# Kernel tuning notes

Measured on AMD Instinct MI355X. Metric: run time of the kernel, lower is better.

## Reference

```python
import jax, jax.numpy as jnp
import numpy as np

FM = 32          # feature_maps
OUT_BITS = 16    # output_bits
PASS_STEPS = 3
N_EDGES = 3_200_000
VAR_COUNT = 100_000
CONST_COUNT = 50_000
EPS = 1e-5       # torch LayerNorm default


def _ln(x):
    # LayerNorm over last dim, elementwise_affine=False
    mu = jnp.mean(x, axis=-1, keepdims=True)
    var = jnp.mean((x - mu) ** 2, axis=-1, keepdims=True)
    return (x - mu) / jnp.sqrt(var + EPS)


def _mlp_ln(x, W1, b1, W2, b2):
    # Linear -> ReLU -> Linear -> LayerNorm(no affine)
    return _ln(jax.nn.relu(x @ W1 + b1) @ W2 + b2)


def _linear_init(key, fan_in, fan_out):
    kW, kb = jax.random.split(key)
    bound = 1.0 / np.sqrt(fan_in)
    W = jax.random.uniform(kW, (fan_in, fan_out), jnp.float32, -bound, bound)
    b = jax.random.uniform(kb, (fan_out,), jnp.float32, -bound, bound)
    return W, b


def setup_inputs() -> dict:
    key = jax.random.key(0)
    ks = jax.random.split(key, 12)
    inp = {}
    inp["edge_var"] = jax.random.randint(ks[0], (N_EDGES,), 0, VAR_COUNT, dtype=jnp.int64 if jax.config.jax_enable_x64 else jnp.int32)
    inp["edge_const"] = jax.random.randint(ks[1], (N_EDGES,), 0, CONST_COUNT, dtype=jnp.int64 if jax.config.jax_enable_x64 else jnp.int32)
    inp["edge_val"] = jax.random.normal(ks[2], (N_EDGES,), jnp.float32)
    inp["conditions_values"] = jax.random.normal(ks[3], (CONST_COUNT,), jnp.float32)
    inp["var_count"] = VAR_COUNT
    inp["const_count"] = CONST_COUNT
    # prepare_cond: 1 -> 2*fm -> fm
    inp["pc_W1"], inp["pc_b1"] = _linear_init(ks[4], 1, 2 * FM)
    inp["pc_W2"], inp["pc_b2"] = _linear_init(ks[5], 2 * FM, FM)
    # constraint_update: 3*fm -> 2*fm -> fm
    inp["cu_W1"], inp["cu_b1"] = _linear_init(ks[6], 3 * FM, 2 * FM)
    inp["cu_W2"], inp["cu_b2"] = _linear_init(ks[7], 2 * FM, FM)
    # variable_update: 2*fm -> 2*fm -> fm
    inp["vu_W1"], inp["vu_b1"] = _linear_init(ks[8], 2 * FM, 2 * FM)
    inp["vu_W2"], inp["vu_b2"] = _linear_init(ks[9], 2 * FM, FM)
    # output: fm -> 2*fm -> output_bits
    inp["out_W1"], inp["out_b1"] = _linear_init(ks[10], FM, 2 * FM)
    inp["out_W2"], inp["out_b2"] = _linear_init(ks[11], 2 * FM, OUT_BITS)
    return inp


def reference(edge_var, edge_const, edge_val, conditions_values, var_count, const_count,
              pc_W1, pc_b1, pc_W2, pc_b2,
              cu_W1, cu_b1, cu_W2, cu_b2,
              vu_W1, vu_b1, vu_W2, vu_b2,
              out_W1, out_b1, out_W2, out_b2):
    variables = jnp.ones((var_count, FM), dtype=edge_val.dtype)
    emb = _mlp_ln(conditions_values[:, None], pc_W1, pc_b1, pc_W2, pc_b2)  # [C, fm]
    constraints = emb
    ev = edge_val[:, None]
    for _ in range(PASS_STEPS):
        # adj.T @ variables : scatter-add variable features into constraints
        v2c = jax.ops.segment_sum(variables[edge_var] * ev, edge_const, num_segments=const_count)
        constraints = _mlp_ln(jnp.concatenate([constraints, emb, v2c], axis=-1),
                              cu_W1, cu_b1, cu_W2, cu_b2)
        # adj @ constraints : scatter-add constraint features into variables
        c2v = jax.ops.segment_sum(constraints[edge_const] * ev, edge_var, num_segments=var_count)
        variables = _mlp_ln(jnp.concatenate([variables, c2v], axis=-1),
                            vu_W1, vu_b1, vu_W2, vu_b2)
    out = jax.nn.relu(variables @ out_W1 + out_b1) @ out_W2 + out_b2
    return jax.nn.sigmoid(out)
```

## Files before the change

### kernel.cpp

```cpp
#include <hip/hip_runtime.h>
#include <hip/hip_fp16.h>
#include <math.h>

#define FM 32
#define N_EDGES 3200000
#define VAR_COUNT 100000
#define CONST_COUNT 50000
#define LN_EPS 1e-5f

#define EPB 4096
#define ABLK 782
#define NB 782
#define AB2 784
#define LSTRIDE 784
#define CAP 4608

typedef _Float16 f16;
typedef __attribute__((ext_vector_type(4))) _Float16 f16x4;
typedef __attribute__((ext_vector_type(4))) float f32x4;

static __device__ __forceinline__ float warp_sum32(float v) {
#pragma unroll
    for (int m = 16; m; m >>= 1) v += __shfl_xor(v, m);
    return v;
}

__global__ void init_vars(float* __restrict__ v, __half* __restrict__ v16, int n) {
    int i = blockIdx.x * 256 + threadIdx.x;
    if (i < n) {
        if (v) v[i] = 1.0f;
        if (v16) v16[i] = __float2half(1.0f);
    }
}


template <int DSHIFT>
__global__ __launch_bounds__(256) void bucket_sort(
    const int* __restrict__ dest_arr, const int* __restrict__ src_arr,
    const float* __restrict__ val_arr,
    int2* __restrict__ recs_tmp, int* __restrict__ lscan, int* __restrict__ rlen_T,
    int n) {
    __shared__ int hist[NB];
    __shared__ int cursor[NB];
    __shared__ int chunk[256];
    __shared__ int2 stage[EPB];
    const int t = threadIdx.x;
    const int base = blockIdx.x * EPB;
    const int nb = min(EPB, n - base);
    for (int i = t; i < NB; i += 256) hist[i] = 0;
    __syncthreads();
    int dg[16], pk[16], vb[16];
#pragma unroll
    for (int k = 0; k < 16; ++k) {
        int j = k * 256 + t;
        dg[k] = -1;
        if (j < nb) {
            int dest = dest_arr[base + j];
            int src  = src_arr[base + j];
            vb[k] = __float_as_int(val_arr[base + j]);
            dg[k] = dest >> DSHIFT;
            pk[k] = ((dest & ((1 << DSHIFT) - 1)) << 20) | src;
            atomicAdd(&hist[dg[k]], 1);
        }
    }
    __syncthreads();
    int sum = 0;
#pragma unroll
    for (int k = 0; k < 4; ++k) {
        int idx = t * 4 + k;
        if (idx < NB) sum += hist[idx];
    }
    chunk[t] = sum;
    __syncthreads();
    for (int off = 1; off < 256; off <<= 1) {
        int v = (t >= off) ? chunk[t - off] : 0;
        __syncthreads();
        chunk[t] += v;
        __syncthreads();
    }
    int run = chunk[t] - sum;
#pragma unroll
    for (int k = 0; k < 4; ++k) {
        int idx = t * 4 + k;
        if (idx < NB) {
            int h = hist[idx];
            rlen_T[(size_t)idx * AB2 + blockIdx.x] = h;
            hist[idx] = run;
            cursor[idx] = run;
            run += h;
        }
    }
    __syncthreads();
    {
        int* lp = lscan + (size_t)blockIdx.x * LSTRIDE;
        for (int i = t; i < NB; i += 256) lp[i] = hist[i];
        if (t == 0) lp[NB] = nb;
    }
#pragma unroll
    for (int k = 0; k < 16; ++k) {
        if (dg[k] >= 0) {
            int pos = atomicAdd(&cursor[dg[k]], 1);
            stage[pos] = make_int2(pk[k], vb[k]);
        }
    }
    __syncthreads();
    for (int j = t; j < nb; j += 256) recs_tmp[(size_t)base + j] = stage[j];
}

__global__ __launch_bounds__(256) void row_sum(const int* __restrict__ rlen_T,
                                               int* __restrict__ btot) {
    __shared__ int ls[256];
    const int t = threadIdx.x;
    const int* rp = rlen_T + (size_t)blockIdx.x * AB2;
    int s = 0;
    for (int b = t; b < ABLK; b += 256) s += rp[b];
    ls[t] = s;
    __syncthreads();
    for (int off = 128; off; off >>= 1) {
        if (t < off) ls[t] += ls[t + off];
        __syncthreads();
    }
    if (t == 0) btot[blockIdx.x] = ls[0];
}

__global__ __launch_bounds__(256) void scan_btot(
    const int* __restrict__ btot, int* __restrict__ bb, int n, int total) {
    __shared__ int ls[256];
    const int t = threadIdx.x;
    int idx = t * 4;
    int a0 = (idx + 0 < n) ? btot[idx + 0] : 0;
    int a1 = (idx + 1 < n) ? btot[idx + 1] : 0;
    int a2 = (idx + 2 < n) ? btot[idx + 2] : 0;
    int a3 = (idx + 3 < n) ? btot[idx + 3] : 0;
    int tsum = a0 + a1 + a2 + a3;
    ls[t] = tsum;
    __syncthreads();
    for (int off = 1; off < 256; off <<= 1) {
        int v = (t >= off) ? ls[t - off] : 0;
        __syncthreads();
        ls[t] += v;
        __syncthreads();
    }
    int excl = ls[t] - tsum;
    if (idx + 0 < n) bb[idx + 0] = excl;
    if (idx + 1 < n) bb[idx + 1] = excl + a0;
    if (idx + 2 < n) bb[idx + 2] = excl + a0 + a1;
    if (idx + 3 < n) bb[idx + 3] = excl + a0 + a1 + a2;
    if (t == 0) bb[n] = total;
}


template <int DSHIFT, int NDEST>
__global__ __launch_bounds__(256) void collect_sort(
    const int2* __restrict__ recs_tmp, const int* __restrict__ lscan,
    const int* __restrict__ rlen_T, const int* __restrict__ bb,
    int2* __restrict__ recs_out, int* __restrict__ offs,
    float* __restrict__ wsum, int nrows) {
    __shared__ int2 stage[CAP];
    __shared__ int rloff[256];
    __shared__ int hist[NDEST];
    __shared__ int cursor[NDEST];
    __shared__ int sc[NDEST];
    __shared__ float wsumL[NDEST];
    __shared__ int nb_s;
    const int t = threadIdx.x;
    const int k = blockIdx.x;
    const int b0 = t * 4;
    int s0 = 0, s1 = 0, s2 = 0, s3 = 0, l0 = 0, l1 = 0, l2 = 0, l3 = 0;
    if (b0 + 0 < ABLK) { s0 = lscan[(size_t)(b0 + 0) * LSTRIDE + k]; l0 = rlen_T[(size_t)k * AB2 + b0 + 0]; }
    if (b0 + 1 < ABLK) { s1 = lscan[(size_t)(b0 + 1) * LSTRIDE + k]; l1 = rlen_T[(size_t)k * AB2 + b0 + 1]; }
    if (b0 + 2 < ABLK) { s2 = lscan[(size_t)(b0 + 2) * LSTRIDE + k]; l2 = rlen_T[(size_t)k * AB2 + b0 + 2]; }
    if (b0 + 3 < ABLK) { s3 = lscan[(size_t)(b0 + 3) * LSTRIDE + k]; l3 = rlen_T[(size_t)k * AB2 + b0 + 3]; }
    int tsum = l0 + l1 + l2 + l3;
    rloff[t] = tsum;
    __syncthreads();
    for (int off = 1; off < 256; off <<= 1) {
        int v = (t >= off) ? rloff[t - off] : 0;
        __syncthreads();
        rloff[t] += v;
        __syncthreads();
    }
    if (t == 255) nb_s = rloff[255];
    int o0 = rloff[t] - tsum;
    int o1 = o0 + l0, o2 = o1 + l1, o3 = o2 + l2;
    for (int i = t; i < NDEST; i += 256) { hist[i] = 0; wsumL[i] = 0.0f; }
    __syncthreads();
    const int nb = min(nb_s, CAP);
    {
        const int2* rp = recs_tmp + (size_t)(b0 + 0) * EPB + s0;
        for (int j = 0; j < l0; ++j) if (o0 + j < CAP) stage[o0 + j] = rp[j];
        rp = recs_tmp + (size_t)(b0 + 1) * EPB + s1;
        for (int j = 0; j < l1; ++j) if (o1 + j < CAP) stage[o1 + j] = rp[j];
        rp = recs_tmp + (size_t)(b0 + 2) * EPB + s2;
        for (int j = 0; j < l2; ++j) if (o2 + j < CAP) stage[o2 + j] = rp[j];
        rp = recs_tmp + (size_t)(b0 + 3) * EPB + s3;
        for (int j = 0; j < l3; ++j) if (o3 + j < CAP) stage[o3 + j] = rp[j];
    }
    __syncthreads();
    for (int j = t; j < nb; j += 256) {
        int2 r = stage[j];
        atomicAdd(&hist[r.x >> 20], 1);
        if (wsum) atomicAdd(&wsumL[r.x >> 20], __int_as_float(r.y));
    }
    __syncthreads();
    if (t < NDEST) sc[t] = hist[t];
    __syncthreads();
    for (int off = 1; off < NDEST; off <<= 1) {
        int v = (t >= off && t < NDEST) ? sc[t - off] : 0;
        __syncthreads();
        if (t < NDEST) sc[t] += v;
        __syncthreads();
    }
    if (t < NDEST) {
        int excl = sc[t] - hist[t];
        cursor[t] = excl;
        int gd = (k << DSHIFT) + t;
        if (gd <= nrows) offs[gd] = bb[k] + excl;
        if (wsum && gd < nrows) wsum[gd] = wsumL[t];
    }
    __syncthreads();
    const int base_out = bb[k];
    for (int j = t; j < nb; j += 256) {
        int2 r = stage[j];
        int pos = atomicAdd(&cursor[r.x >> 20], 1);
        recs_out[(size_t)base_out + pos] = make_int2(r.x & 0xFFFFF, r.y);
    }
}


__global__ __launch_bounds__(256) void seg_gather16(
    const int* __restrict__ offs, const int2* __restrict__ recs,
    const __half* __restrict__ src16, __half* __restrict__ dst16, int nrows) {
    const int g = threadIdx.x >> 4, f2 = threadIdx.x & 15;
    const int row = blockIdx.x * 16 + g;
    if (row >= nrows) return;
    int j = offs[row];
    const int j1 = offs[row + 1];
    const __half2* __restrict__ s2 = (const __half2*)src16;
    float ax[8], ay[8];
#pragma unroll
    for (int u = 0; u < 8; ++u) { ax[u] = 0.0f; ay[u] = 0.0f; }
    for (; j + 8 <= j1; j += 8) {
        int2 r[8];
#pragma unroll
        for (int u = 0; u < 8; ++u) r[u] = recs[j + u];
        __half2 hh[8];
#pragma unroll
        for (int u = 0; u < 8; ++u) hh[u] = s2[(size_t)r[u].x * 16 + f2];
#pragma unroll
        for (int u = 0; u < 8; ++u) {
            float w = __int_as_float(r[u].y);
            float2 f = __half22float2(hh[u]);
            ax[u] = fmaf(f.x, w, ax[u]);
            ay[u] = fmaf(f.y, w, ay[u]);
        }
    }
    for (; j < j1; ++j) {
        int2 ra = recs[j];
        __half2 ha = s2[(size_t)ra.x * 16 + f2];
        float wa = __int_as_float(ra.y);
        float2 fa = __half22float2(ha);
        ax[0] = fmaf(fa.x, wa, ax[0]);
        ay[0] = fmaf(fa.y, wa, ay[0]);
    }
    float rx = ((ax[0] + ax[1]) + (ax[2] + ax[3])) + ((ax[4] + ax[5]) + (ax[6] + ax[7]));
    float ry = ((ay[0] + ay[1]) + (ay[2] + ay[3])) + ((ay[4] + ay[5]) + (ay[6] + ay[7]));
    ((__half2*)dst16)[(size_t)row * 16 + f2] = __floats2half2_rn(rx, ry);
}


__global__ __launch_bounds__(256) void scatter_edges(
    const int* __restrict__ src_idx, const int* __restrict__ dst_idx,
    const float* __restrict__ ev, const float* __restrict__ src,
    float* __restrict__ dst, int n_edges) {
    int e = blockIdx.x * 8 + (threadIdx.x >> 5);
    int f = threadIdx.x & 31;
    if (e >= n_edges) return;
    atomicAdd(&dst[(size_t)dst_idx[e] * FM + f], src[(size_t)src_idx[e] * FM + f] * ev[e]);
}


template <int NSEG>
__global__ __launch_bounds__(256) void mlp_mfma(
    const __half* __restrict__ s0h, const __half* __restrict__ s1h,
    const __half* __restrict__ s2h, const float* __restrict__ ws,
    const float* __restrict__ W1, const float* __restrict__ b1,
    const float* __restrict__ W2, const float* __restrict__ b2,
    __half* __restrict__ dst16, int nrows) {
    constexpr int KT = NSEG * 2;
    __shared__ float hbuf[4][16][68];
    const int t = threadIdx.x;
    const int w = t >> 6;
    const int L = t & 63;
    const int c = L & 15;
    const int g = L >> 4;
    f16x4 B1[KT * 4];
#pragma unroll
    for (int kt = 0; kt < KT; ++kt) {
#pragma unroll
        for (int jt = 0; jt < 4; ++jt) {
            f16x4 bf;
#pragma unroll
            for (int i = 0; i < 4; ++i)
                bf[i] = (f16)W1[(size_t)(kt * 16 + 4 * g + i) * 64 + jt * 16 + c];
            B1[kt * 4 + jt] = bf;
        }
    }
    f16x4 B2[8];
#pragma unroll
    for (int kt = 0; kt < 4; ++kt) {
#pragma unroll
        for (int ct = 0; ct < 2; ++ct) {
            f16x4 bf;
#pragma unroll
            for (int i = 0; i < 4; ++i)
                bf[i] = (f16)W2[(size_t)(kt * 16 + 4 * g + i) * 32 + ct * 16 + c];
            B2[kt * 2 + ct] = bf;
        }
    }
    float b1v[4];
#pragma unroll
    for (int jt = 0; jt < 4; ++jt) b1v[jt] = b1[jt * 16 + c];
    const float b2v0 = b2[c], b2v1 = b2[16 + c];
    const f16* sa0 = (const f16*)s0h;
    const f16* sa1 = (const f16*)s1h;
    const f16* sa2 = (const f16*)s2h;

    const int step = gridDim.x * 4 * 16;
    for (int r0 = (blockIdx.x * 4 + w) * 16; r0 < nrows; r0 += step) {
        const int arow = r0 + c;
        f32x4 C1[4];
#pragma unroll
        for (int jt = 0; jt < 4; ++jt) {
            C1[jt][0] = 0.0f; C1[jt][1] = 0.0f; C1[jt][2] = 0.0f; C1[jt][3] = 0.0f;
        }
        f16x4 wsfrag;
        if (NSEG == 3 && ws) {
            f16 wv = (f16)ws[arow];
            wsfrag[0] = wv; wsfrag[1] = wv; wsfrag[2] = wv; wsfrag[3] = wv;
        }
#pragma unroll
        for (int kt = 0; kt < KT; ++kt) {
            f16x4 a;
            if (NSEG == 3 && kt >= 4 && ws) {
                a = wsfrag;
            } else {
                const f16* sp = (kt < 2) ? sa0 : ((kt < 4) ? sa1 : sa2);
                a = *(const f16x4*)(sp + (size_t)arow * FM + (kt & 1) * 16 + 4 * g);
            }
#pragma unroll
            for (int jt = 0; jt < 4; ++jt)
                C1[jt] = __builtin_amdgcn_mfma_f32_16x16x16f16(a, B1[kt * 4 + jt],
                                                               C1[jt], 0, 0, 0);
        }
#pragma unroll
        for (int jt = 0; jt < 4; ++jt)
#pragma unroll
            for (int j = 0; j < 4; ++j)
                hbuf[w][4 * g + j][jt * 16 + c] = fmaxf(C1[jt][j] + b1v[jt], 0.0f);
        asm volatile("s_waitcnt lgkmcnt(0)" ::: "memory");
        f16x4 A2[4];
#pragma unroll
        for (int kt = 0; kt < 4; ++kt) {
            float4 hv = *(const float4*)&hbuf[w][c][kt * 16 + 4 * g];
            f16x4 af;
            af[0] = (f16)hv.x; af[1] = (f16)hv.y; af[2] = (f16)hv.z; af[3] = (f16)hv.w;
            A2[kt] = af;
        }
        f32x4 C2[2];
        C2[0][0] = 0.0f; C2[0][1] = 0.0f; C2[0][2] = 0.0f; C2[0][3] = 0.0f;
        C2[1][0] = 0.0f; C2[1][1] = 0.0f; C2[1][2] = 0.0f; C2[1][3] = 0.0f;
#pragma unroll
        for (int kt = 0; kt < 4; ++kt) {
            C2[0] = __builtin_amdgcn_mfma_f32_16x16x16f16(A2[kt], B2[kt * 2 + 0],
                                                          C2[0], 0, 0, 0);
            C2[1] = __builtin_amdgcn_mfma_f32_16x16x16f16(A2[kt], B2[kt * 2 + 1],
                                                          C2[1], 0, 0, 0);
        }
#pragma unroll
        for (int j = 0; j < 4; ++j) {
            float y0 = C2[0][j] + b2v0;
            float y1 = C2[1][j] + b2v1;
            float s = y0 + y1;
            s += __shfl_xor(s, 1); s += __shfl_xor(s, 2);
            s += __shfl_xor(s, 4); s += __shfl_xor(s, 8);
            float mu = s * (1.0f / 32.0f);
            float d0 = y0 - mu, d1 = y1 - mu;
            float q = d0 * d0 + d1 * d1;
            q += __shfl_xor(q, 1); q += __shfl_xor(q, 2);
            q += __shfl_xor(q, 4); q += __shfl_xor(q, 8);
            float rs = rsqrtf(q * (1.0f / 32.0f) + LN_EPS);
            const size_t rbase = (size_t)(r0 + 4 * g + j) * FM;
            dst16[rbase + c]      = __float2half(d0 * rs);
            dst16[rbase + 16 + c] = __float2half(d1 * rs);
        }
    }
}


__global__ __launch_bounds__(256) void pc_mlp(
    const float* __restrict__ cond,
    const float* __restrict__ W1, const float* __restrict__ b1,
    const float* __restrict__ W2, const float* __restrict__ b2,
    float* __restrict__ dstA, float* __restrict__ dstB,
    __half* __restrict__ dstA16, __half* __restrict__ dstB16, int nrows) {
    __shared__ float sW2[64 * FM];
    __shared__ float sh[4][64];
    for (int i = threadIdx.x; i < 64 * FM; i += 256) sW2[i] = W2[i];
    int g = threadIdx.x >> 6, l = threadIdx.x & 63, l32 = l & 31, half = l >> 5;
    float w1l = W1[l], b1l = b1[l], b2l = b2[l32];
    __syncthreads();
    for (int row = blockIdx.x * 4 + g; row < nrows; row += gridDim.x * 4) {
        float cc = cond[row];
        sh[g][l] = fmaxf(fmaf(cc, w1l, b1l), 0.0f);
        float y = 0.0f;
#pragma unroll
        for (int k = 0; k < 32; k += 4) {
            float4 hv = *(const float4*)&sh[g][half * 32 + k];
            y = fmaf(hv.x, sW2[(half * 32 + k + 0) * FM + l32], y);
            y = fmaf(hv.y, sW2[(half * 32 + k + 1) * FM + l32], y);
            y = fmaf(hv.z, sW2[(half * 32 + k + 2) * FM + l32], y);
            y = fmaf(hv.w, sW2[(half * 32 + k + 3) * FM + l32], y);
        }
        y += __shfl_xor(y, 32);
        y += b2l;
        float s = warp_sum32(y);
        float mu = s * (1.0f / 32.0f);
        float d = y - mu;
        float v = warp_sum32(d * d);
        if (half == 0) {
            float o = d * rsqrtf(v * (1.0f / 32.0f) + LN_EPS);
            if (dstA)   dstA[(size_t)row * FM + l32] = o;
            if (dstB)   dstB[(size_t)row * FM + l32] = o;
            if (dstA16) dstA16[(size_t)row * FM + l32] = __float2half(o);
            if (dstB16) dstB16[(size_t)row * FM + l32] = __float2half(o);
        }
    }
}

template <int NSEG>
__global__ __launch_bounds__(256) void mlp_ln_f32(
    const float* __restrict__ s0, const float* __restrict__ s1,
    const float* __restrict__ s2,
    const float* __restrict__ W1, const float* __restrict__ b1,
    const float* __restrict__ W2, const float* __restrict__ b2,
    float* __restrict__ dst, __half* __restrict__ dst16, int nrows) {
    constexpr int IN = NSEG * FM;
    __shared__ float sW2[64 * FM];
    __shared__ float sx[4][IN];
    __shared__ float sh[4][64];
    for (int i = threadIdx.x; i < 64 * FM; i += 256) sW2[i] = W2[i];
    int g = threadIdx.x >> 6, l = threadIdx.x & 63, l32 = l & 31, half = l >> 5;
    float w1r[IN];
#pragma unroll
    for (int k = 0; k < IN; ++k) w1r[k] = W1[k * 64 + l];
    float b1l = b1[l], b2l = b2[l32];
    __syncthreads();
    for (int row = blockIdx.x * 4 + g; row < nrows; row += gridDim.x * 4) {
#pragma unroll
        for (int i = l; i < IN; i += 64) {
            const float* s = (i < 32) ? s0 : (i < 64) ? s1 : s2;
            sx[g][i] = s[(size_t)row * FM + (i & 31)];
        }
        float acc = b1l;
#pragma unroll
        for (int k = 0; k < IN; k += 4) {
            float4 xv = *(const float4*)&sx[g][k];
            acc = fmaf(xv.x, w1r[k + 0], acc);
            acc = fmaf(xv.y, w1r[k + 1], acc);
            acc = fmaf(xv.z, w1r[k + 2], acc);
            acc = fmaf(xv.w, w1r[k + 3], acc);
        }
        sh[g][l] = fmaxf(acc, 0.0f);
        float y = 0.0f;
#pragma unroll
        for (int k = 0; k < 32; k += 4) {
            float4 hv = *(const float4*)&sh[g][half * 32 + k];
            y = fmaf(hv.x, sW2[(half * 32 + k + 0) * FM + l32], y);
            y = fmaf(hv.y, sW2[(half * 32 + k + 1) * FM + l32], y);
            y = fmaf(hv.z, sW2[(half * 32 + k + 2) * FM + l32], y);
            y = fmaf(hv.w, sW2[(half * 32 + k + 3) * FM + l32], y);
        }
        y += __shfl_xor(y, 32);
        y += b2l;
        float s = warp_sum32(y);
        float mu = s * (1.0f / 32.0f);
        float d = y - mu;
        float v = warp_sum32(d * d);
        if (half == 0) {
            float o = d * rsqrtf(v * (1.0f / 32.0f) + LN_EPS);
            dst[(size_t)row * FM + l32] = o;
            if (dst16) dst16[(size_t)row * FM + l32] = __float2half(o);
        }
    }
}

__global__ __launch_bounds__(256) void out_mlp(
    const __half* __restrict__ x16,
    const float* __restrict__ W1, const float* __restrict__ b1,
    const float* __restrict__ W2, const float* __restrict__ b2,
    float* __restrict__ dst, int nrows) {
    __shared__ float sW2[64 * 16];
    __shared__ float sx[4][FM];
    __shared__ float sh[4][64];
    for (int i = threadIdx.x; i < 64 * 16; i += 256) sW2[i] = W2[i];
    int g = threadIdx.x >> 6, l = threadIdx.x & 63;
    int o = l & 15, q = l >> 4;
    float w1r[FM];
#pragma unroll
    for (int k = 0; k < FM; ++k) w1r[k] = W1[k * 64 + l];
    float b1l = b1[l];
    float b2o = b2[o];
    __syncthreads();
    for (int row = blockIdx.x * 4 + g; row < nrows; row += gridDim.x * 4) {
        if (l < FM) sx[g][l] = __half2float(x16[(size_t)row * FM + l]);
        float acc = b1l;
#pragma unroll
        for (int k = 0; k < FM; k += 4) {
            float4 xv = *(const float4*)&sx[g][k];
            acc = fmaf(xv.x, w1r[k + 0], acc);
            acc = fmaf(xv.y, w1r[k + 1], acc);
            acc = fmaf(xv.z, w1r[k + 2], acc);
            acc = fmaf(xv.w, w1r[k + 3], acc);
        }
        sh[g][l] = fmaxf(acc, 0.0f);
        float y = 0.0f;
#pragma unroll
        for (int k = 0; k < 16; k += 4) {
            int kk = q * 16 + k;
            float4 hv = *(const float4*)&sh[g][kk];
            y = fmaf(hv.x, sW2[(kk + 0) * 16 + o], y);
            y = fmaf(hv.y, sW2[(kk + 1) * 16 + o], y);
            y = fmaf(hv.z, sW2[(kk + 2) * 16 + o], y);
            y = fmaf(hv.w, sW2[(kk + 3) * 16 + o], y);
        }
        y += __shfl_xor(y, 16);
        y += __shfl_xor(y, 32);
        if (q == 0) dst[(size_t)row * 16 + o] = 1.0f / (1.0f + expf(-(y + b2o)));
    }
}


extern "C" void kernel_launch(void* const* d_in, const int* in_sizes, int n_in,
                              void* d_out, int out_size, void* d_ws, size_t ws_size,
                              hipStream_t stream) {
    const int*   edge_var   = (const int*)d_in[0];
    const int*   edge_const = (const int*)d_in[1];
    const float* edge_val   = (const float*)d_in[2];
    const float* cond       = (const float*)d_in[3];
    const float* pc_W1 = (const float*)d_in[6];
    const float* pc_b1 = (const float*)d_in[7];
    const float* pc_W2 = (const float*)d_in[8];
    const float* pc_b2 = (const float*)d_in[9];
    const float* cu_W1 = (const float*)d_in[10];
    const float* cu_b1 = (const float*)d_in[11];
    const float* cu_W2 = (const float*)d_in[12];
    const float* cu_b2 = (const float*)d_in[13];
    const float* vu_W1 = (const float*)d_in[14];
    const float* vu_b1 = (const float*)d_in[15];
    const float* vu_W2 = (const float*)d_in[16];
    const float* vu_b2 = (const float*)d_in[17];
    const float* out_W1 = (const float*)d_in[18];
    const float* out_b1 = (const float*)d_in[19];
    const float* out_W2 = (const float*)d_in[20];
    const float* out_b2 = (const float*)d_in[21];

    float* ws = (float*)d_ws;
    size_t off = 0;
    auto alloc = [&](size_t nelems) {
        float* p = ws + off;
        off += (nelems + 15) & ~(size_t)15;
        return p;
    };
    __half* vars16 = (__half*)alloc(VAR_COUNT * FM / 2);
    __half* cons16 = (__half*)alloc(CONST_COUNT * FM / 2);
    __half* emb16  = (__half*)alloc(CONST_COUNT * FM / 2);
    __half* msg16  = (__half*)alloc(VAR_COUNT * FM / 2);
    int2*   recs_t = (int2*)alloc((size_t)N_EDGES * 2);
    int2*   recs_c = (int2*)alloc((size_t)N_EDGES * 2);
    int2*   recs_v = (int2*)alloc((size_t)N_EDGES * 2);
    int*    lscan  = (int*)alloc((size_t)ABLK * LSTRIDE);
    int*    rlen_T = (int*)alloc((size_t)NB * AB2);
    int*    btot   = (int*)alloc(NB);
    int*    bb_c   = (int*)alloc(NB + 1);
    int*    bb_v   = (int*)alloc(NB + 1);
    int*    offs_c = (int*)alloc(CONST_COUNT + 1);
    int*    offs_v = (int*)alloc(VAR_COUNT + 1);
    float*  wsum_c = alloc(CONST_COUNT);
    size_t need_bytes = off * sizeof(float);
    bool fast = ws_size >= need_bytes;

    float* emb  = (float*)recs_t;
    float* cons = emb + CONST_COUNT * FM;
    float* vars = cons + CONST_COUNT * FM;
    float* msg  = (float*)recs_c;

    if (fast) {
        bucket_sort<6><<<ABLK, 256, 0, stream>>>(edge_const, edge_var, edge_val,
                                                 recs_t, lscan, rlen_T, N_EDGES);
        row_sum<<<NB, 256, 0, stream>>>(rlen_T, btot);
        scan_btot<<<1, 256, 0, stream>>>(btot, bb_c, NB, N_EDGES);
        collect_sort<6, 64><<<NB, 256, 0, stream>>>(recs_t, lscan, rlen_T, bb_c,
                                                    recs_c, offs_c, wsum_c, CONST_COUNT);
        bucket_sort<7><<<ABLK, 256, 0, stream>>>(edge_var, edge_const, edge_val,
                                                 recs_t, lscan, rlen_T, N_EDGES);
        row_sum<<<NB, 256, 0, stream>>>(rlen_T, btot);
        scan_btot<<<1, 256, 0, stream>>>(btot, bb_v, NB, N_EDGES);
        collect_sort<7, 128><<<NB, 256, 0, stream>>>(recs_t, lscan, rlen_T, bb_v,
                                                     recs_v, offs_v, nullptr, VAR_COUNT);

        init_vars<<<(VAR_COUNT * FM + 255) / 256, 256, 0, stream>>>(
            nullptr, vars16, VAR_COUNT * FM);
        pc_mlp<<<1024, 256, 0, stream>>>(cond, pc_W1, pc_b1, pc_W2, pc_b2,
                                         nullptr, nullptr, emb16, cons16, CONST_COUNT);

        for (int pass = 0; pass < 3; ++pass) {
            if (pass == 0) {
                mlp_mfma<3><<<512, 256, 0, stream>>>(
                    cons16, emb16, nullptr, wsum_c,
                    cu_W1, cu_b1, cu_W2, cu_b2, cons16, CONST_COUNT);
            } else {
                seg_gather16<<<(CONST_COUNT + 15) / 16, 256, 0, stream>>>(
                    offs_c, recs_c, vars16, msg16, CONST_COUNT);
                mlp_mfma<3><<<512, 256, 0, stream>>>(
                    cons16, emb16, msg16, nullptr,
                    cu_W1, cu_b1, cu_W2, cu_b2, cons16, CONST_COUNT);
            }
            seg_gather16<<<(VAR_COUNT + 15) / 16, 256, 0, stream>>>(
                offs_v, recs_v, cons16, msg16, VAR_COUNT);
            mlp_mfma<2><<<512, 256, 0, stream>>>(
                vars16, msg16, nullptr, nullptr,
                vu_W1, vu_b1, vu_W2, vu_b2, vars16, VAR_COUNT);
        }
    } else {
        init_vars<<<(VAR_COUNT * FM + 255) / 256, 256, 0, stream>>>(
            vars, vars16, VAR_COUNT * FM);
        pc_mlp<<<1024, 256, 0, stream>>>(cond, pc_W1, pc_b1, pc_W2, pc_b2,
                                         emb, cons, nullptr, nullptr, CONST_COUNT);
        for (int pass = 0; pass < 3; ++pass) {
            hipMemsetAsync(msg, 0, (size_t)CONST_COUNT * FM * sizeof(float), stream);
            scatter_edges<<<N_EDGES / 8, 256, 0, stream>>>(edge_var, edge_const, edge_val,
                                                           vars, msg, N_EDGES);
            mlp_ln_f32<3><<<1024, 256, 0, stream>>>(cons, emb, msg,
                                                    cu_W1, cu_b1, cu_W2, cu_b2,
                                                    cons, nullptr, CONST_COUNT);
            hipMemsetAsync(msg, 0, (size_t)VAR_COUNT * FM * sizeof(float), stream);
            scatter_edges<<<N_EDGES / 8, 256, 0, stream>>>(edge_const, edge_var, edge_val,
                                                           cons, msg, N_EDGES);
            mlp_ln_f32<2><<<1024, 256, 0, stream>>>(vars, msg, nullptr,
                                                    vu_W1, vu_b1, vu_W2, vu_b2,
                                                    vars, vars16, VAR_COUNT);
        }
    }

    out_mlp<<<1024, 256, 0, stream>>>(vars16, out_W1, out_b1, out_W2, out_b2,
                                      (float*)d_out, VAR_COUNT);
}
```

Baseline: 447.9 us.

## Split collect_sort into two half-source blocks per bucket, dropping LDS staging

Each destination bucket's collect_sort now runs as two blocks, each covering half of the source blocks. This doubles the grid, and the kernel reads records directly from global memory instead of staging them in a large LDS buffer. Each half writes its own offsets and weight sums, so seg_gather16 walks two segments per row and mlp_mfma adds the two wsum halves. The intent is more parallelism and occupancy in the sort phase, at the cost of reading records from global memory twice and extra offset loads in each gather pass.

```diff
diff --git a/kernel.cpp b/kernel.cpp
--- a/kernel.cpp
+++ b/kernel.cpp
@@ -10,10 +10,10 @@
 
 #define EPB 4096
 #define ABLK 782
+#define HABLK 391
 #define NB 782
 #define AB2 784
 #define LSTRIDE 784
-#define CAP 4608
 
 typedef _Float16 f16;
 typedef __attribute__((ext_vector_type(4))) _Float16 f16x4;
@@ -111,28 +111,33 @@
                                                int* __restrict__ btot) {
     __shared__ int ls[256];
     const int t = threadIdx.x;
-    const int* rp = rlen_T + (size_t)blockIdx.x * AB2;
+    const int blk = blockIdx.x;
+    const int h = (blk >= NB) ? 1 : 0;
+    const int k = blk - h * NB;
+    const int* rp = rlen_T + (size_t)k * AB2 + h * HABLK;
     int s = 0;
-    for (int b = t; b < ABLK; b += 256) s += rp[b];
+    for (int b = t; b < HABLK; b += 256) s += rp[b];
     ls[t] = s;
     __syncthreads();
     for (int off = 128; off; off >>= 1) {
         if (t < off) ls[t] += ls[t + off];
         __syncthreads();
     }
-    if (t == 0) btot[blockIdx.x] = ls[0];
+    if (t == 0) btot[blk] = ls[0];
 }
 
 __global__ __launch_bounds__(256) void scan_btot(
     const int* __restrict__ btot, int* __restrict__ bb, int n, int total) {
     __shared__ int ls[256];
     const int t = threadIdx.x;
-    int idx = t * 4;
-    int a0 = (idx + 0 < n) ? btot[idx + 0] : 0;
-    int a1 = (idx + 1 < n) ? btot[idx + 1] : 0;
-    int a2 = (idx + 2 < n) ? btot[idx + 2] : 0;
-    int a3 = (idx + 3 < n) ? btot[idx + 3] : 0;
-    int tsum = a0 + a1 + a2 + a3;
+    int a[8];
+    const int idx = t * 8;
+    int tsum = 0;
+#pragma unroll
+    for (int u = 0; u < 8; ++u) {
+        a[u] = (idx + u < n) ? btot[idx + u] : 0;
+        tsum += a[u];
+    }
     ls[t] = tsum;
     __syncthreads();
     for (int off = 1; off < 256; off <<= 1) {
@@ -142,10 +147,11 @@
         __syncthreads();
     }
     int excl = ls[t] - tsum;
-    if (idx + 0 < n) bb[idx + 0] = excl;
-    if (idx + 1 < n) bb[idx + 1] = excl + a0;
-    if (idx + 2 < n) bb[idx + 2] = excl + a0 + a1;
-    if (idx + 3 < n) bb[idx + 3] = excl + a0 + a1 + a2;
+#pragma unroll
+    for (int u = 0; u < 8; ++u) {
+        if (idx + u < n) bb[idx + u] = excl;
+        excl += a[u];
+    }
     if (t == 0) bb[n] = total;
 }
 
@@ -154,53 +160,36 @@
 __global__ __launch_bounds__(256) void collect_sort(
     const int2* __restrict__ recs_tmp, const int* __restrict__ lscan,
     const int* __restrict__ rlen_T, const int* __restrict__ bb,
-    int2* __restrict__ recs_out, int* __restrict__ offs,
-    float* __restrict__ wsum, int nrows) {
-    __shared__ int2 stage[CAP];
-    __shared__ int rloff[256];
+    int2* __restrict__ recs_out, int* __restrict__ offs0, int* __restrict__ offs1,
+    float* __restrict__ wsum0, float* __restrict__ wsum1, int nrows) {
     __shared__ int hist[NDEST];
     __shared__ int cursor[NDEST];
     __shared__ int sc[NDEST];
     __shared__ float wsumL[NDEST];
-    __shared__ int nb_s;
     const int t = threadIdx.x;
-    const int k = blockIdx.x;
-    const int b0 = t * 4;
-    int s0 = 0, s1 = 0, s2 = 0, s3 = 0, l0 = 0, l1 = 0, l2 = 0, l3 = 0;
-    if (b0 + 0 < ABLK) { s0 = lscan[(size_t)(b0 + 0) * LSTRIDE + k]; l0 = rlen_T[(size_t)k * AB2 + b0 + 0]; }
-    if (b0 + 1 < ABLK) { s1 = lscan[(size_t)(b0 + 1) * LSTRIDE + k]; l1 = rlen_T[(size_t)k * AB2 + b0 + 1]; }
-    if (b0 + 2 < ABLK) { s2 = lscan[(size_t)(b0 + 2) * LSTRIDE + k]; l2 = rlen_T[(size_t)k * AB2 + b0 + 2]; }
-    if (b0 + 3 < ABLK) { s3 = lscan[(size_t)(b0 + 3) * LSTRIDE + k]; l3 = rlen_T[(size_t)k * AB2 + b0 + 3]; }
-    int tsum = l0 + l1 + l2 + l3;
-    rloff[t] = tsum;
-    __syncthreads();
-    for (int off = 1; off < 256; off <<= 1) {
-        int v = (t >= off) ? rloff[t - off] : 0;
-        __syncthreads();
-        rloff[t] += v;
-        __syncthreads();
-    }
-    if (t == 255) nb_s = rloff[255];
-    int o0 = rloff[t] - tsum;
-    int o1 = o0 + l0, o2 = o1 + l1, o3 = o2 + l2;
+    const int blk = blockIdx.x;
+    const int h = (blk >= NB) ? 1 : 0;
+    const int k = blk - h * NB;
+    const int bsb = h * HABLK;
+    int* __restrict__ offsH = h ? offs1 : offs0;
+    float* __restrict__ wsumH = (wsum0 == nullptr) ? nullptr : (h ? wsum1 : wsum0);
+    const int c0 = t * 2, c1 = t * 2 + 1;
+    int s0 = 0, l0 = 0, s1 = 0, l1 = 0;
+    if (c0 < HABLK) { s0 = lscan[(size_t)(bsb + c0) * LSTRIDE + k]; l0 = rlen_T[(size_t)k * AB2 + bsb + c0]; }
+    if (c1 < HABLK) { s1 = lscan[(size_t)(bsb + c1) * LSTRIDE + k]; l1 = rlen_T[(size_t)k * AB2 + bsb + c1]; }
+    const int2* rp0 = recs_tmp + (size_t)(bsb + c0) * EPB + s0;
+    const int2* rp1 = recs_tmp + (size_t)(bsb + c1) * EPB + s1;
     for (int i = t; i < NDEST; i += 256) { hist[i] = 0; wsumL[i] = 0.0f; }
     __syncthreads();
-    const int nb = min(nb_s, CAP);
-    {
-        const int2* rp = recs_tmp + (size_t)(b0 + 0) * EPB + s0;
-        for (int j = 0; j < l0; ++j) if (o0 + j < CAP) stage[o0 + j] = rp[j];
-        rp = recs_tmp + (size_t)(b0 + 1) * EPB + s1;
-        for (int j = 0; j < l1; ++j) if (o1 + j < CAP) stage[o1 + j] = rp[j];
-        rp = recs_tmp + (size_t)(b0 + 2) * EPB + s2;
-        for (int j = 0; j < l2; ++j) if (o2 + j < CAP) stage[o2 + j] = rp[j];
-        rp = recs_tmp + (size_t)(b0 + 3) * EPB + s3;
-        for (int j = 0; j < l3; ++j) if (o3 + j < CAP) stage[o3 + j] = rp[j];
-    }
-    __syncthreads();
-    for (int j = t; j < nb; j += 256) {
-        int2 r = stage[j];
+    for (int j = 0; j < l0; ++j) {
+        int2 r = rp0[j];
         atomicAdd(&hist[r.x >> 20], 1);
-        if (wsum) atomicAdd(&wsumL[r.x >> 20], __int_as_float(r.y));
+        if (wsumH) atomicAdd(&wsumL[r.x >> 20], __int_as_float(r.y));
+    }
+    for (int j = 0; j < l1; ++j) {
+        int2 r = rp1[j];
+        atomicAdd(&hist[r.x >> 20], 1);
+        if (wsumH) atomicAdd(&wsumL[r.x >> 20], __int_as_float(r.y));
     }
     __syncthreads();
     if (t < NDEST) sc[t] = hist[t];
@@ -215,53 +204,62 @@
         int excl = sc[t] - hist[t];
         cursor[t] = excl;
         int gd = (k << DSHIFT) + t;
-        if (gd <= nrows) offs[gd] = bb[k] + excl;
-        if (wsum && gd < nrows) wsum[gd] = wsumL[t];
-    }
-    __syncthreads();
-    const int base_out = bb[k];
-    for (int j = t; j < nb; j += 256) {
-        int2 r = stage[j];
+        if (gd <= nrows) offsH[gd] = bb[blk] + excl;
+        if (wsumH && gd < nrows) wsumH[gd] = wsumL[t];
+    }
+    __syncthreads();
+    const int base_out = bb[blk];
+    for (int j = 0; j < l0; ++j) {
+        int2 r = rp0[j];
         int pos = atomicAdd(&cursor[r.x >> 20], 1);
         recs_out[(size_t)base_out + pos] = make_int2(r.x & 0xFFFFF, r.y);
     }
+    for (int j = 0; j < l1; ++j) {
+        int2 r = rp1[j];
+        int pos = atomicAdd(&cursor[r.x >> 20], 1);
+        recs_out[(size_t)base_out + pos] = make_int2(r.x & 0xFFFFF, r.y);
+    }
 }
 
 
 __global__ __launch_bounds__(256) void seg_gather16(
-    const int* __restrict__ offs, const int2* __restrict__ recs,
+    const int* __restrict__ offs0, const int* __restrict__ offs1,
+    const int2* __restrict__ recs,
     const __half* __restrict__ src16, __half* __restrict__ dst16, int nrows) {
     const int g = threadIdx.x >> 4, f2 = threadIdx.x & 15;
     const int row = blockIdx.x * 16 + g;
     if (row >= nrows) return;
-    int j = offs[row];
-    const int j1 = offs[row + 1];
     const __half2* __restrict__ s2 = (const __half2*)src16;
     float ax[8], ay[8];
 #pragma unroll
     for (int u = 0; u < 8; ++u) { ax[u] = 0.0f; ay[u] = 0.0f; }
-    for (; j + 8 <= j1; j += 8) {
-        int2 r[8];
-#pragma unroll
-        for (int u = 0; u < 8; ++u) r[u] = recs[j + u];
-        __half2 hh[8];
-#pragma unroll
-        for (int u = 0; u < 8; ++u) hh[u] = s2[(size_t)r[u].x * 16 + f2];
-#pragma unroll
-        for (int u = 0; u < 8; ++u) {
-            float w = __int_as_float(r[u].y);
-            float2 f = __half22float2(hh[u]);
-            ax[u] = fmaf(f.x, w, ax[u]);
-            ay[u] = fmaf(f.y, w, ay[u]);
-        }
-    }
-    for (; j < j1; ++j) {
-        int2 ra = recs[j];
-        __half2 ha = s2[(size_t)ra.x * 16 + f2];
-        float wa = __int_as_float(ra.y);
-        float2 fa = __half22float2(ha);
-        ax[0] = fmaf(fa.x, wa, ax[0]);
-        ay[0] = fmaf(fa.y, wa, ay[0]);
+    for (int h = 0; h < 2; ++h) {
+        const int* __restrict__ of = h ? offs1 : offs0;
+        int j = of[row];
+        const int j1 = of[row + 1];
+        for (; j + 8 <= j1; j += 8) {
+            int2 r[8];
+#pragma unroll
+            for (int u = 0; u < 8; ++u) r[u] = recs[j + u];
+            __half2 hh[8];
+#pragma unroll
+            for (int u = 0; u < 8; ++u) hh[u] = s2[(size_t)r[u].x * 16 + f2];
+#pragma unroll
+            for (int u = 0; u < 8; ++u) {
+                float w = __int_as_float(r[u].y);
+                float2 f = __half22float2(hh[u]);
+                ax[u] = fmaf(f.x, w, ax[u]);
+                ay[u] = fmaf(f.y, w, ay[u]);
+            }
+        }
+        for (; j < j1; ++j) {
+            int2 ra = recs[j];
+            __half2 ha = s2[(size_t)ra.x * 16 + f2];
+            float wa = __int_as_float(ra.y);
+            float2 fa = __half22float2(ha);
+            ax[0] = fmaf(fa.x, wa, ax[0]);
+            ay[0] = fmaf(fa.y, wa, ay[0]);
+        }
     }
     float rx = ((ax[0] + ax[1]) + (ax[2] + ax[3])) + ((ax[4] + ax[5]) + (ax[6] + ax[7]));
     float ry = ((ay[0] + ay[1]) + (ay[2] + ay[3])) + ((ay[4] + ay[5]) + (ay[6] + ay[7]));
@@ -283,7 +281,8 @@
 template <int NSEG>
 __global__ __launch_bounds__(256) void mlp_mfma(
     const __half* __restrict__ s0h, const __half* __restrict__ s1h,
-    const __half* __restrict__ s2h, const float* __restrict__ ws,
+    const __half* __restrict__ s2h,
+    const float* __restrict__ ws0, const float* __restrict__ ws1,
     const float* __restrict__ W1, const float* __restrict__ b1,
     const float* __restrict__ W2, const float* __restrict__ b2,
     __half* __restrict__ dst16, int nrows) {
@@ -335,14 +334,14 @@
             C1[jt][0] = 0.0f; C1[jt][1] = 0.0f; C1[jt][2] = 0.0f; C1[jt][3] = 0.0f;
         }
         f16x4 wsfrag;
-        if (NSEG == 3 && ws) {
-            f16 wv = (f16)ws[arow];
+        if (NSEG == 3 && ws0) {
+            f16 wv = (f16)(ws0[arow] + ws1[arow]);
             wsfrag[0] = wv; wsfrag[1] = wv; wsfrag[2] = wv; wsfrag[3] = wv;
         }
 #pragma unroll
         for (int kt = 0; kt < KT; ++kt) {
             f16x4 a;
-            if (NSEG == 3 && kt >= 4 && ws) {
+            if (NSEG == 3 && kt >= 4 && ws0) {
                 a = wsfrag;
             } else {
                 const f16* sp = (kt < 2) ? sa0 : ((kt < 4) ? sa1 : sa2);
@@ -572,21 +571,24 @@
         off += (nelems + 15) & ~(size_t)15;
         return p;
     };
-    __half* vars16 = (__half*)alloc(VAR_COUNT * FM / 2);
-    __half* cons16 = (__half*)alloc(CONST_COUNT * FM / 2);
-    __half* emb16  = (__half*)alloc(CONST_COUNT * FM / 2);
-    __half* msg16  = (__half*)alloc(VAR_COUNT * FM / 2);
-    int2*   recs_t = (int2*)alloc((size_t)N_EDGES * 2);
-    int2*   recs_c = (int2*)alloc((size_t)N_EDGES * 2);
-    int2*   recs_v = (int2*)alloc((size_t)N_EDGES * 2);
-    int*    lscan  = (int*)alloc((size_t)ABLK * LSTRIDE);
-    int*    rlen_T = (int*)alloc((size_t)NB * AB2);
-    int*    btot   = (int*)alloc(NB);
-    int*    bb_c   = (int*)alloc(NB + 1);
-    int*    bb_v   = (int*)alloc(NB + 1);
-    int*    offs_c = (int*)alloc(CONST_COUNT + 1);
-    int*    offs_v = (int*)alloc(VAR_COUNT + 1);
-    float*  wsum_c = alloc(CONST_COUNT);
+    __half* vars16  = (__half*)alloc(VAR_COUNT * FM / 2);
+    __half* cons16  = (__half*)alloc(CONST_COUNT * FM / 2);
+    __half* emb16   = (__half*)alloc(CONST_COUNT * FM / 2);
+    __half* msg16   = (__half*)alloc(VAR_COUNT * FM / 2);
+    int2*   recs_t  = (int2*)alloc((size_t)N_EDGES * 2);
+    int2*   recs_c  = (int2*)alloc((size_t)N_EDGES * 2);
+    int2*   recs_v  = (int2*)alloc((size_t)N_EDGES * 2);
+    int*    lscan   = (int*)alloc((size_t)ABLK * LSTRIDE);
+    int*    rlen_T  = (int*)alloc((size_t)NB * AB2);
+    int*    btot    = (int*)alloc(2 * NB);
+    int*    bb_c    = (int*)alloc(2 * NB + 1);
+    int*    bb_v    = (int*)alloc(2 * NB + 1);
+    int*    offs_c0 = (int*)alloc(CONST_COUNT + 1);
+    int*    offs_c1 = (int*)alloc(CONST_COUNT + 1);
+    int*    offs_v0 = (int*)alloc(VAR_COUNT + 1);
+    int*    offs_v1 = (int*)alloc(VAR_COUNT + 1);
+    float*  wsum_c0 = alloc(CONST_COUNT);
+    float*  wsum_c1 = alloc(CONST_COUNT);
     size_t need_bytes = off * sizeof(float);
     bool fast = ws_size >= need_bytes;
 
@@ -598,16 +600,18 @@
     if (fast) {
         bucket_sort<6><<<ABLK, 256, 0, stream>>>(edge_const, edge_var, edge_val,
                                                  recs_t, lscan, rlen_T, N_EDGES);
-        row_sum<<<NB, 256, 0, stream>>>(rlen_T, btot);
-        scan_btot<<<1, 256, 0, stream>>>(btot, bb_c, NB, N_EDGES);
-        collect_sort<6, 64><<<NB, 256, 0, stream>>>(recs_t, lscan, rlen_T, bb_c,
-                                                    recs_c, offs_c, wsum_c, CONST_COUNT);
+        row_sum<<<2 * NB, 256, 0, stream>>>(rlen_T, btot);
+        scan_btot<<<1, 256, 0, stream>>>(btot, bb_c, 2 * NB, N_EDGES);
+        collect_sort<6, 64><<<2 * NB, 256, 0, stream>>>(
+            recs_t, lscan, rlen_T, bb_c, recs_c, offs_c0, offs_c1,
+            wsum_c0, wsum_c1, CONST_COUNT);
         bucket_sort<7><<<ABLK, 256, 0, stream>>>(edge_var, edge_const, edge_val,
                                                  recs_t, lscan, rlen_T, N_EDGES);
-        row_sum<<<NB, 256, 0, stream>>>(rlen_T, btot);
-        scan_btot<<<1, 256, 0, stream>>>(btot, bb_v, NB, N_EDGES);
-        collect_sort<7, 128><<<NB, 256, 0, stream>>>(recs_t, lscan, rlen_T, bb_v,
-                                                     recs_v, offs_v, nullptr, VAR_COUNT);
+        row_sum<<<2 * NB, 256, 0, stream>>>(rlen_T, btot);
+        scan_btot<<<1, 256, 0, stream>>>(btot, bb_v, 2 * NB, N_EDGES);
+        collect_sort<7, 128><<<2 * NB, 256, 0, stream>>>(
+            recs_t, lscan, rlen_T, bb_v, recs_v, offs_v0, offs_v1,
+            nullptr, nullptr, VAR_COUNT);
 
         init_vars<<<(VAR_COUNT * FM + 255) / 256, 256, 0, stream>>>(
             nullptr, vars16, VAR_COUNT * FM);
@@ -617,19 +621,19 @@
         for (int pass = 0; pass < 3; ++pass) {
             if (pass == 0) {
                 mlp_mfma<3><<<512, 256, 0, stream>>>(
-                    cons16, emb16, nullptr, wsum_c,
+                    cons16, emb16, nullptr, wsum_c0, wsum_c1,
                     cu_W1, cu_b1, cu_W2, cu_b2, cons16, CONST_COUNT);
             } else {
                 seg_gather16<<<(CONST_COUNT + 15) / 16, 256, 0, stream>>>(
-                    offs_c, recs_c, vars16, msg16, CONST_COUNT);
+                    offs_c0, offs_c1, recs_c, vars16, msg16, CONST_COUNT);
                 mlp_mfma<3><<<512, 256, 0, stream>>>(
-                    cons16, emb16, msg16, nullptr,
+                    cons16, emb16, msg16, nullptr, nullptr,
                     cu_W1, cu_b1, cu_W2, cu_b2, cons16, CONST_COUNT);
             }
             seg_gather16<<<(VAR_COUNT + 15) / 16, 256, 0, stream>>>(
-                offs_v, recs_v, cons16, msg16, VAR_COUNT);
+                offs_v0, offs_v1, recs_v, cons16, msg16, VAR_COUNT);
             mlp_mfma<2><<<512, 256, 0, stream>>>(
-                vars16, msg16, nullptr, nullptr,
+                vars16, msg16, nullptr, nullptr, nullptr,
                 vu_W1, vu_b1, vu_W2, vu_b2, vars16, VAR_COUNT);
         }
     } else {
```

Result: slower. 505.3 us (+12.8%).

## Double bucket count in two-pass edge sort and store local scans transposed

Applied to the files above, without the earlier changes.

The CSR bucket sort now uses about twice as many coarse buckets (1563 instead of 782), so each collect block handles half as many edges with a smaller shared stage. It also drops the separate cursor array, and writes per-block bucket scan offsets transposed so collect_sort reads them contiguously. Separately, the segmented gather gains a 16-way unrolled inner loop to get more gather loads in flight. The costs are larger histograms and prefix scans per block and more collect blocks; a capacity overflow is possible if a coarse bucket exceeds the smaller 2560-entry stage.

```diff
diff --git a/kernel.cpp b/kernel.cpp
--- a/kernel.cpp
+++ b/kernel.cpp
@@ -10,10 +10,10 @@
 
 #define EPB 4096
 #define ABLK 782
-#define NB 782
+#define NBUCK 1563
+#define BPT 7
 #define AB2 784
-#define LSTRIDE 784
-#define CAP 4608
+#define CAPH 2560
 
 typedef _Float16 f16;
 typedef __attribute__((ext_vector_type(4))) _Float16 f16x4;
@@ -38,16 +38,15 @@
 __global__ __launch_bounds__(256) void bucket_sort(
     const int* __restrict__ dest_arr, const int* __restrict__ src_arr,
     const float* __restrict__ val_arr,
-    int2* __restrict__ recs_tmp, int* __restrict__ lscan, int* __restrict__ rlen_T,
+    int2* __restrict__ recs_tmp, int* __restrict__ lscan_T, int* __restrict__ rlen_T,
     int n) {
-    __shared__ int hist[NB];
-    __shared__ int cursor[NB];
+    __shared__ int hist[NBUCK];
     __shared__ int chunk[256];
     __shared__ int2 stage[EPB];
     const int t = threadIdx.x;
     const int base = blockIdx.x * EPB;
     const int nb = min(EPB, n - base);
-    for (int i = t; i < NB; i += 256) hist[i] = 0;
+    for (int i = t; i < NBUCK; i += 256) hist[i] = 0;
     __syncthreads();
     int dg[16], pk[16], vb[16];
 #pragma unroll
@@ -66,9 +65,9 @@
     __syncthreads();
     int sum = 0;
 #pragma unroll
-    for (int k = 0; k < 4; ++k) {
-        int idx = t * 4 + k;
-        if (idx < NB) sum += hist[idx];
+    for (int k = 0; k < BPT; ++k) {
+        int idx = t * BPT + k;
+        if (idx < NBUCK) sum += hist[idx];
     }
     chunk[t] = sum;
     __syncthreads();
@@ -80,26 +79,21 @@
     }
     int run = chunk[t] - sum;
 #pragma unroll
-    for (int k = 0; k < 4; ++k) {
-        int idx = t * 4 + k;
-        if (idx < NB) {
+    for (int k = 0; k < BPT; ++k) {
+        int idx = t * BPT + k;
+        if (idx < NBUCK) {
             int h = hist[idx];
             rlen_T[(size_t)idx * AB2 + blockIdx.x] = h;
+            lscan_T[(size_t)idx * AB2 + blockIdx.x] = run;
             hist[idx] = run;
-            cursor[idx] = run;
             run += h;
         }
     }
     __syncthreads();
-    {
-        int* lp = lscan + (size_t)blockIdx.x * LSTRIDE;
-        for (int i = t; i < NB; i += 256) lp[i] = hist[i];
-        if (t == 0) lp[NB] = nb;
-    }
 #pragma unroll
     for (int k = 0; k < 16; ++k) {
         if (dg[k] >= 0) {
-            int pos = atomicAdd(&cursor[dg[k]], 1);
+            int pos = atomicAdd(&hist[dg[k]], 1);
             stage[pos] = make_int2(pk[k], vb[k]);
         }
     }
@@ -127,12 +121,14 @@
     const int* __restrict__ btot, int* __restrict__ bb, int n, int total) {
     __shared__ int ls[256];
     const int t = threadIdx.x;
-    int idx = t * 4;
-    int a0 = (idx + 0 < n) ? btot[idx + 0] : 0;
-    int a1 = (idx + 1 < n) ? btot[idx + 1] : 0;
-    int a2 = (idx + 2 < n) ? btot[idx + 2] : 0;
-    int a3 = (idx + 3 < n) ? btot[idx + 3] : 0;
-    int tsum = a0 + a1 + a2 + a3;
+    int a[8];
+    const int idx = t * 8;
+    int tsum = 0;
+#pragma unroll
+    for (int u = 0; u < 8; ++u) {
+        a[u] = (idx + u < n) ? btot[idx + u] : 0;
+        tsum += a[u];
+    }
     ls[t] = tsum;
     __syncthreads();
     for (int off = 1; off < 256; off <<= 1) {
@@ -142,24 +138,24 @@
         __syncthreads();
     }
     int excl = ls[t] - tsum;
-    if (idx + 0 < n) bb[idx + 0] = excl;
-    if (idx + 1 < n) bb[idx + 1] = excl + a0;
-    if (idx + 2 < n) bb[idx + 2] = excl + a0 + a1;
-    if (idx + 3 < n) bb[idx + 3] = excl + a0 + a1 + a2;
+#pragma unroll
+    for (int u = 0; u < 8; ++u) {
+        if (idx + u < n) bb[idx + u] = excl;
+        excl += a[u];
+    }
     if (t == 0) bb[n] = total;
 }
 
 
 template <int DSHIFT, int NDEST>
 __global__ __launch_bounds__(256) void collect_sort(
-    const int2* __restrict__ recs_tmp, const int* __restrict__ lscan,
+    const int2* __restrict__ recs_tmp, const int* __restrict__ lscan_T,
     const int* __restrict__ rlen_T, const int* __restrict__ bb,
     int2* __restrict__ recs_out, int* __restrict__ offs,
     float* __restrict__ wsum, int nrows) {
-    __shared__ int2 stage[CAP];
+    __shared__ int2 stage[CAPH];
     __shared__ int rloff[256];
     __shared__ int hist[NDEST];
-    __shared__ int cursor[NDEST];
     __shared__ int sc[NDEST];
     __shared__ float wsumL[NDEST];
     __shared__ int nb_s;
@@ -167,10 +163,10 @@
     const int k = blockIdx.x;
     const int b0 = t * 4;
     int s0 = 0, s1 = 0, s2 = 0, s3 = 0, l0 = 0, l1 = 0, l2 = 0, l3 = 0;
-    if (b0 + 0 < ABLK) { s0 = lscan[(size_t)(b0 + 0) * LSTRIDE + k]; l0 = rlen_T[(size_t)k * AB2 + b0 + 0]; }
-    if (b0 + 1 < ABLK) { s1 = lscan[(size_t)(b0 + 1) * LSTRIDE + k]; l1 = rlen_T[(size_t)k * AB2 + b0 + 1]; }
-    if (b0 + 2 < ABLK) { s2 = lscan[(size_t)(b0 + 2) * LSTRIDE + k]; l2 = rlen_T[(size_t)k * AB2 + b0 + 2]; }
-    if (b0 + 3 < ABLK) { s3 = lscan[(size_t)(b0 + 3) * LSTRIDE + k]; l3 = rlen_T[(size_t)k * AB2 + b0 + 3]; }
+    if (b0 + 0 < ABLK) { s0 = lscan_T[(size_t)k * AB2 + b0 + 0]; l0 = rlen_T[(size_t)k * AB2 + b0 + 0]; }
+    if (b0 + 1 < ABLK) { s1 = lscan_T[(size_t)k * AB2 + b0 + 1]; l1 = rlen_T[(size_t)k * AB2 + b0 + 1]; }
+    if (b0 + 2 < ABLK) { s2 = lscan_T[(size_t)k * AB2 + b0 + 2]; l2 = rlen_T[(size_t)k * AB2 + b0 + 2]; }
+    if (b0 + 3 < ABLK) { s3 = lscan_T[(size_t)k * AB2 + b0 + 3]; l3 = rlen_T[(size_t)k * AB2 + b0 + 3]; }
     int tsum = l0 + l1 + l2 + l3;
     rloff[t] = tsum;
     __syncthreads();
@@ -185,16 +181,16 @@
     int o1 = o0 + l0, o2 = o1 + l1, o3 = o2 + l2;
     for (int i = t; i < NDEST; i += 256) { hist[i] = 0; wsumL[i] = 0.0f; }
     __syncthreads();
-    const int nb = min(nb_s, CAP);
+    const int nb = min(nb_s, CAPH);
     {
         const int2* rp = recs_tmp + (size_t)(b0 + 0) * EPB + s0;
-        for (int j = 0; j < l0; ++j) if (o0 + j < CAP) stage[o0 + j] = rp[j];
+        for (int j = 0; j < l0; ++j) if (o0 + j < CAPH) stage[o0 + j] = rp[j];
         rp = recs_tmp + (size_t)(b0 + 1) * EPB + s1;
-        for (int j = 0; j < l1; ++j) if (o1 + j < CAP) stage[o1 + j] = rp[j];
+        for (int j = 0; j < l1; ++j) if (o1 + j < CAPH) stage[o1 + j] = rp[j];
         rp = recs_tmp + (size_t)(b0 + 2) * EPB + s2;
-        for (int j = 0; j < l2; ++j) if (o2 + j < CAP) stage[o2 + j] = rp[j];
+        for (int j = 0; j < l2; ++j) if (o2 + j < CAPH) stage[o2 + j] = rp[j];
         rp = recs_tmp + (size_t)(b0 + 3) * EPB + s3;
-        for (int j = 0; j < l3; ++j) if (o3 + j < CAP) stage[o3 + j] = rp[j];
+        for (int j = 0; j < l3; ++j) if (o3 + j < CAPH) stage[o3 + j] = rp[j];
     }
     __syncthreads();
     for (int j = t; j < nb; j += 256) {
@@ -213,16 +209,16 @@
     }
     if (t < NDEST) {
         int excl = sc[t] - hist[t];
-        cursor[t] = excl;
         int gd = (k << DSHIFT) + t;
         if (gd <= nrows) offs[gd] = bb[k] + excl;
         if (wsum && gd < nrows) wsum[gd] = wsumL[t];
+        hist[t] = excl;
     }
     __syncthreads();
     const int base_out = bb[k];
     for (int j = t; j < nb; j += 256) {
         int2 r = stage[j];
-        int pos = atomicAdd(&cursor[r.x >> 20], 1);
+        int pos = atomicAdd(&hist[r.x >> 20], 1);
         recs_out[(size_t)base_out + pos] = make_int2(r.x & 0xFFFFF, r.y);
     }
 }
@@ -240,6 +236,21 @@
     float ax[8], ay[8];
 #pragma unroll
     for (int u = 0; u < 8; ++u) { ax[u] = 0.0f; ay[u] = 0.0f; }
+    for (; j + 16 <= j1; j += 16) {
+        int2 r[16];
+#pragma unroll
+        for (int u = 0; u < 16; ++u) r[u] = recs[j + u];
+        __half2 hh[16];
+#pragma unroll
+        for (int u = 0; u < 16; ++u) hh[u] = s2[(size_t)r[u].x * 16 + f2];
+#pragma unroll
+        for (int u = 0; u < 16; ++u) {
+            float w = __int_as_float(r[u].y);
+            float2 f = __half22float2(hh[u]);
+            ax[u & 7] = fmaf(f.x, w, ax[u & 7]);
+            ay[u & 7] = fmaf(f.y, w, ay[u & 7]);
+        }
+    }
     for (; j + 8 <= j1; j += 8) {
         int2 r[8];
 #pragma unroll
@@ -572,21 +583,21 @@
         off += (nelems + 15) & ~(size_t)15;
         return p;
     };
-    __half* vars16 = (__half*)alloc(VAR_COUNT * FM / 2);
-    __half* cons16 = (__half*)alloc(CONST_COUNT * FM / 2);
-    __half* emb16  = (__half*)alloc(CONST_COUNT * FM / 2);
-    __half* msg16  = (__half*)alloc(VAR_COUNT * FM / 2);
-    int2*   recs_t = (int2*)alloc((size_t)N_EDGES * 2);
-    int2*   recs_c = (int2*)alloc((size_t)N_EDGES * 2);
-    int2*   recs_v = (int2*)alloc((size_t)N_EDGES * 2);
-    int*    lscan  = (int*)alloc((size_t)ABLK * LSTRIDE);
-    int*    rlen_T = (int*)alloc((size_t)NB * AB2);
-    int*    btot   = (int*)alloc(NB);
-    int*    bb_c   = (int*)alloc(NB + 1);
-    int*    bb_v   = (int*)alloc(NB + 1);
-    int*    offs_c = (int*)alloc(CONST_COUNT + 1);
-    int*    offs_v = (int*)alloc(VAR_COUNT + 1);
-    float*  wsum_c = alloc(CONST_COUNT);
+    __half* vars16  = (__half*)alloc(VAR_COUNT * FM / 2);
+    __half* cons16  = (__half*)alloc(CONST_COUNT * FM / 2);
+    __half* emb16   = (__half*)alloc(CONST_COUNT * FM / 2);
+    __half* msg16   = (__half*)alloc(VAR_COUNT * FM / 2);
+    int2*   recs_t  = (int2*)alloc((size_t)N_EDGES * 2);
+    int2*   recs_c  = (int2*)alloc((size_t)N_EDGES * 2);
+    int2*   recs_v  = (int2*)alloc((size_t)N_EDGES * 2);
+    int*    lscan_T = (int*)alloc((size_t)NBUCK * AB2);
+    int*    rlen_T  = (int*)alloc((size_t)NBUCK * AB2);
+    int*    btot    = (int*)alloc(NBUCK);
+    int*    bb_c    = (int*)alloc(NBUCK + 1);
+    int*    bb_v    = (int*)alloc(NBUCK + 1);
+    int*    offs_c  = (int*)alloc(CONST_COUNT + 1);
+    int*    offs_v  = (int*)alloc(VAR_COUNT + 1);
+    float*  wsum_c  = alloc(CONST_COUNT);
     size_t need_bytes = off * sizeof(float);
     bool fast = ws_size >= need_bytes;
 
@@ -596,18 +607,18 @@
     float* msg  = (float*)recs_c;
 
     if (fast) {
-        bucket_sort<6><<<ABLK, 256, 0, stream>>>(edge_const, edge_var, edge_val,
-                                                 recs_t, lscan, rlen_T, N_EDGES);
-        row_sum<<<NB, 256, 0, stream>>>(rlen_T, btot);
-        scan_btot<<<1, 256, 0, stream>>>(btot, bb_c, NB, N_EDGES);
-        collect_sort<6, 64><<<NB, 256, 0, stream>>>(recs_t, lscan, rlen_T, bb_c,
-                                                    recs_c, offs_c, wsum_c, CONST_COUNT);
-        bucket_sort<7><<<ABLK, 256, 0, stream>>>(edge_var, edge_const, edge_val,
-                                                 recs_t, lscan, rlen_T, N_EDGES);
-        row_sum<<<NB, 256, 0, stream>>>(rlen_T, btot);
-        scan_btot<<<1, 256, 0, stream>>>(btot, bb_v, NB, N_EDGES);
-        collect_sort<7, 128><<<NB, 256, 0, stream>>>(recs_t, lscan, rlen_T, bb_v,
-                                                     recs_v, offs_v, nullptr, VAR_COUNT);
+        bucket_sort<5><<<ABLK, 256, 0, stream>>>(edge_const, edge_var, edge_val,
+                                                 recs_t, lscan_T, rlen_T, N_EDGES);
+        row_sum<<<NBUCK, 256, 0, stream>>>(rlen_T, btot);
+        scan_btot<<<1, 256, 0, stream>>>(btot, bb_c, NBUCK, N_EDGES);
+        collect_sort<5, 32><<<NBUCK, 256, 0, stream>>>(
+            recs_t, lscan_T, rlen_T, bb_c, recs_c, offs_c, wsum_c, CONST_COUNT);
+        bucket_sort<6><<<ABLK, 256, 0, stream>>>(edge_var, edge_const, edge_val,
+                                                 recs_t, lscan_T, rlen_T, N_EDGES);
+        row_sum<<<NBUCK, 256, 0, stream>>>(rlen_T, btot);
+        scan_btot<<<1, 256, 0, stream>>>(btot, bb_v, NBUCK, N_EDGES);
+        collect_sort<6, 64><<<NBUCK, 256, 0, stream>>>(
+            recs_t, lscan_T, rlen_T, bb_v, recs_v, offs_v, nullptr, VAR_COUNT);
 
         init_vars<<<(VAR_COUNT * FM + 255) / 256, 256, 0, stream>>>(
             nullptr, vars16, VAR_COUNT * FM);
```

Measured after the change: 469.8 us. +4.9%, slower.
